# Kernel tuning notes

Hardware: AMD Instinct MI355X
Metric: run time of the kernel (lower is better)

Reference implementation:

```python
import jax, jax.numpy as jnp
import numpy as np

D_IN, N_HEADS, HEAD_DIM = 2048, 16, 128
SEQ, BATCH = 2048, 1
EPS = 1e-6


def rms_norm(x, scale, shift):
    # matches torch RMSNorm: computed in fp32, (1+scale)*x_norm + shift, cast back
    xf = x.astype(jnp.float32)
    rms = jnp.sqrt(jnp.mean(xf * xf, axis=-1, keepdims=True) + EPS)
    out = (xf / rms) * (1.0 + scale.astype(jnp.float32)) + shift.astype(jnp.float32)
    return out.astype(x.dtype)


def apply_rope(x, sin_t, cos_t):
    # x: [b, h, s, d]; sin/cos: [s, d]
    d = x.shape[-1]
    x1, x2 = x[..., : d // 2], x[..., d // 2 :]
    rot = jnp.concatenate([-x2, x1], axis=-1)
    return (x * cos_t[None, None] + rot * sin_t[None, None]).astype(x.dtype)


def setup_inputs() -> dict:
    key = jax.random.key(0)
    ks = jax.random.split(key, 8)
    x = jax.random.normal(ks[0], (BATCH, SEQ, D_IN), dtype=jnp.float32)
    # causal mask: True above the diagonal (positions to mask)
    mask = jnp.triu(jnp.ones((SEQ, SEQ), dtype=bool), k=1)
    # standard RoPE tables, shape [s, head_dim] (half-freqs tiled over both halves)
    inv_freq = 1.0 / (10000.0 ** (np.arange(0, HEAD_DIM, 2, dtype=np.float32) / HEAD_DIM))
    t = np.arange(SEQ, dtype=np.float32)
    ang = np.einsum('s,f->sf', t, inv_freq)          # [s, d/2]
    ang = np.concatenate([ang, ang], axis=-1)        # [s, d]
    sin_thetas = jnp.asarray(np.sin(ang))
    cos_thetas = jnp.asarray(np.cos(ang))
    d_out = N_HEADS * HEAD_DIM
    std = 0.02
    w_q = jax.random.normal(ks[1], (d_out, D_IN), dtype=jnp.float32) * std
    w_k = jax.random.normal(ks[2], (HEAD_DIM, D_IN), dtype=jnp.float32) * std
    w_v = jax.random.normal(ks[3], (HEAD_DIM, D_IN), dtype=jnp.float32) * std
    w_o = jax.random.normal(ks[4], (D_IN, d_out), dtype=jnp.float32) * std
    q_scale = jnp.zeros((HEAD_DIM,), jnp.float32)
    q_shift = jnp.zeros((HEAD_DIM,), jnp.float32)
    k_scale = jnp.zeros((HEAD_DIM,), jnp.float32)
    k_shift = jnp.zeros((HEAD_DIM,), jnp.float32)
    return dict(x=x, mask=mask, sin_thetas=sin_thetas, cos_thetas=cos_thetas,
                w_q=w_q, w_k=w_k, w_v=w_v, w_o=w_o,
                q_scale=q_scale, q_shift=q_shift, k_scale=k_scale, k_shift=k_shift)


def reference(x, mask, sin_thetas, cos_thetas, w_q, w_k, w_v, w_o,
              q_scale, q_shift, k_scale, k_shift):
    b, s, _ = x.shape
    scale = HEAD_DIM ** -0.5
    q = jnp.einsum('bsd,ed->bse', x, w_q).reshape(b, s, N_HEADS, HEAD_DIM)
    q = jnp.transpose(q, (0, 2, 1, 3))                 # [b, H, s, Dh]
    k = jnp.einsum('bsd,ed->bse', x, w_k)[:, None]     # [b, 1, s, Dh]
    v = jnp.einsum('bsd,ed->bse', x, w_v)[:, None]     # [b, 1, s, Dh]
    q = rms_norm(q, q_scale, q_shift)
    k = rms_norm(k, k_scale, k_shift)
    q = apply_rope(q, sin_thetas, cos_thetas)
    k = apply_rope(k, sin_thetas, cos_thetas)
    # MQA: broadcast single K/V head instead of repeat_interleave
    scores = jnp.einsum('bhqd,bokd->bhqk', q, k) * scale   # o==1 broadcast
    scores = jnp.where(mask[None, None], -jnp.inf, scores)
    w = jax.nn.softmax(scores, axis=-1)
    out = jnp.einsum('bhqk,bokd->bhqd', w, v)
    out = jnp.transpose(out, (0, 2, 1, 3)).reshape(b, s, N_HEADS * HEAD_DIM)
    return jnp.einsum('bse,de->bsd', out, w_o)
```

## Files before the change

kernel.cpp:

```cpp
#include <hip/hip_runtime.h>
#include <stdint.h>

#define SEQ 2048
#define DIN 2048
#define NH 16
#define HD 128

typedef __attribute__((ext_vector_type(8))) short bf16x8;
typedef __attribute__((ext_vector_type(4))) float f32x4;

__device__ __forceinline__ unsigned short f2bf(float f) {
    unsigned int u = __float_as_uint(f);
    u += 0x7fff + ((u >> 16) & 1);
    return (unsigned short)(u >> 16);
}

__device__ __forceinline__ float bf2f(unsigned short u) {
    return __uint_as_float(((unsigned int)u) << 16);
}

__device__ __forceinline__ void gload_lds16(const void* g, void* l) {
    __builtin_amdgcn_global_load_lds(
        (const __attribute__((address_space(1))) unsigned int*)g,
        (__attribute__((address_space(3))) unsigned int*)l,
        16, 0, 0);
}

__global__ void cast_f32_bf16(const float* __restrict__ in, unsigned short* __restrict__ out, int n) {
    int i = (blockIdx.x * blockDim.x + threadIdx.x) * 4;
    if (i >= n) return;
    float4 v = *reinterpret_cast<const float4*>(in + i);
    ushort4 o;
    o.x = f2bf(v.x); o.y = f2bf(v.y); o.z = f2bf(v.z); o.w = f2bf(v.w);
    *reinterpret_cast<ushort4*>(out + i) = o;
}

template<int OUT_MODE>
__launch_bounds__(256)
__global__ void gemm_bt(const unsigned short* __restrict__ A,
                        const unsigned short* __restrict__ B,
                        void* __restrict__ Cv, int M, int N, int K) {
    __shared__ __align__(16) unsigned short As[128 * 32];
    __shared__ __align__(16) unsigned short Bs[128 * 32];
    const int t = threadIdx.x;
    const int l = t & 63;
    const int w = t >> 6;
    const int wr = w >> 1, wc = w & 1;
    const int row0 = blockIdx.y * 128, col0 = blockIdx.x * 128;
    const int lr = l & 15, lk = (l >> 4) * 8;

    f32x4 acc[4][4] = {};

    const unsigned short* Ag0 = A + (size_t)(row0 + t / 4) * K + (t % 4) * 8;
    const unsigned short* Ag1 = Ag0 + (size_t)64 * K;
    const unsigned short* Bg0 = B + (size_t)(col0 + t / 4) * K + (t % 4) * 8;
    const unsigned short* Bg1 = Bg0 + (size_t)64 * K;

    for (int k0 = 0; k0 < K; k0 += 32) {
        gload_lds16(Ag0 + k0, &As[t * 8]);
        gload_lds16(Ag1 + k0, &As[2048 + t * 8]);
        gload_lds16(Bg0 + k0, &Bs[t * 8]);
        gload_lds16(Bg1 + k0, &Bs[2048 + t * 8]);
        __syncthreads();
        bf16x8 af[4], bfr[4];
#pragma unroll
        for (int m = 0; m < 4; ++m)
            af[m] = *reinterpret_cast<const bf16x8*>(&As[(wr * 64 + m * 16 + lr) * 32 + lk]);
#pragma unroll
        for (int n = 0; n < 4; ++n)
            bfr[n] = *reinterpret_cast<const bf16x8*>(&Bs[(wc * 64 + n * 16 + lr) * 32 + lk]);
#pragma unroll
        for (int m = 0; m < 4; ++m)
#pragma unroll
            for (int n = 0; n < 4; ++n)
                acc[m][n] = __builtin_amdgcn_mfma_f32_16x16x32_bf16(af[m], bfr[n], acc[m][n], 0, 0, 0);
        __syncthreads();
    }

#pragma unroll
    for (int m = 0; m < 4; ++m) {
        int row_b = row0 + wr * 64 + m * 16 + (l >> 4) * 4;
#pragma unroll
        for (int n = 0; n < 4; ++n) {
            int col = col0 + wc * 64 + n * 16 + lr;
#pragma unroll
            for (int jr = 0; jr < 4; ++jr) {
                int row = row_b + jr;
                if (OUT_MODE == 0)
                    ((float*)Cv)[(size_t)row * N + col] = acc[m][n][jr];
                else if (OUT_MODE == 1)
                    ((unsigned short*)Cv)[(size_t)row * N + col] = f2bf(acc[m][n][jr]);
                else
                    ((unsigned short*)Cv)[(size_t)col * M + row] = f2bf(acc[m][n][jr]);
            }
        }
    }
}

__global__ void norm_rope(const unsigned short* __restrict__ in, int srow,
                          unsigned short* __restrict__ out,
                          const float* __restrict__ sin_t, const float* __restrict__ cos_t,
                          const float* __restrict__ scale, const float* __restrict__ shift,
                          int nh) {
    int w = threadIdx.x >> 6, lane = threadIdx.x & 63;
    int vec = blockIdx.x * 4 + w;
    if (vec >= SEQ * nh) return;
    int s = vec / nh, hh = vec % nh;
    const unsigned short* base = in + (size_t)s * srow + hh * HD;
    float x1 = bf2f(base[lane]), x2 = bf2f(base[lane + 64]);
    float ss = x1 * x1 + x2 * x2;
#pragma unroll
    for (int off = 1; off < 64; off <<= 1) ss += __shfl_xor(ss, off, 64);
    float rinv = rsqrtf(ss * (1.0f / 128.0f) + 1e-6f);
    float xn1 = x1 * rinv * (1.0f + scale[lane]) + shift[lane];
    float xn2 = x2 * rinv * (1.0f + scale[lane + 64]) + shift[lane + 64];
    float c1 = cos_t[s * HD + lane], s1 = sin_t[s * HD + lane];
    float c2 = cos_t[s * HD + lane + 64], s2 = sin_t[s * HD + lane + 64];
    float o1 = xn1 * c1 - xn2 * s1;
    float o2 = xn2 * c2 + xn1 * s2;
    out[(size_t)vec * HD + lane] = f2bf(o1);
    out[(size_t)vec * HD + lane + 64] = f2bf(o2);
}

__launch_bounds__(256)
__global__ void flash_attn2(const unsigned short* __restrict__ Q,
                            const unsigned short* __restrict__ Kb,
                            const unsigned short* __restrict__ Vtg,
                            unsigned short* __restrict__ O) {
    __shared__ __align__(16) unsigned short Ks[2][64 * 128];
    __shared__ __align__(16) unsigned short Vs[2][128 * 64];
    __shared__ __align__(16) unsigned short Pl[4][16 * 64];
    const int t = threadIdx.x, l = t & 63, w = t >> 6;
    const int h = blockIdx.y;
    const int lr = l & 15, g = l >> 4, lk = g * 8;
    const float sc = 0.08838834764831845f;

    auto stage = [&](int buf, int k0) {
#pragma unroll
        for (int i = 0; i < 4; ++i) {
            int c = w * 256 + i * 64 + l;
            int kr = c >> 4, kc = c & 15;
            gload_lds16(Kb + (size_t)(k0 + kr) * HD + ((kc ^ (kr & 7)) * 8),
                        &Ks[buf][c * 8]);
            int vd = c >> 3, vc = c & 7;
            gload_lds16(Vtg + (size_t)vd * SEQ + k0 + ((vc ^ (vd & 7)) * 8),
                        &Vs[buf][c * 8]);
        }
    };

    auto process = [&](int qt) {
        const int q0 = qt * 64;
        bf16x8 qf[4];
        const unsigned short* qbase = Q + (size_t)(q0 + w * 16 + lr) * (NH * HD) + h * HD + lk;
#pragma unroll
        for (int kf = 0; kf < 4; ++kf)
            qf[kf] = *reinterpret_cast<const bf16x8*>(qbase + kf * 32);

        f32x4 acc[8] = {};
        float mrow[4] = {-1e30f, -1e30f, -1e30f, -1e30f};
        float lrow[4] = {0.f, 0.f, 0.f, 0.f};
        const int nt = qt + 1;
        int buf = 0;
        stage(0, 0);
        __syncthreads();

        for (int kt = 0; kt < nt; ++kt) {
            if (kt + 1 < nt) stage(buf ^ 1, (kt + 1) * 64);

            f32x4 s4[4];
#pragma unroll
            for (int nf = 0; nf < 4; ++nf) {
                int row = nf * 16 + lr;
                f32x4 a = {};
#pragma unroll
                for (int kf = 0; kf < 4; ++kf) {
                    bf16x8 kfrag = *reinterpret_cast<const bf16x8*>(
                        &Ks[buf][row * 128 + ((kf * 32 + lk) ^ ((row & 7) << 3))]);
                    a = __builtin_amdgcn_mfma_f32_16x16x32_bf16(qf[kf], kfrag, a, 0, 0, 0);
                }
                s4[nf] = a;
            }

            float sv[4][4];
            const bool diag = (kt == qt);
#pragma unroll
            for (int jr = 0; jr < 4; ++jr)
#pragma unroll
                for (int nf = 0; nf < 4; ++nf) {
                    float x = s4[nf][jr] * sc;
                    if (diag && (nf * 16 + lr > w * 16 + g * 4 + jr)) x = -1e30f;
                    sv[jr][nf] = x;
                }

            float mx[4];
#pragma unroll
            for (int jr = 0; jr < 4; ++jr) {
                float m2 = fmaxf(fmaxf(sv[jr][0], sv[jr][1]), fmaxf(sv[jr][2], sv[jr][3]));
                m2 = fmaxf(m2, __shfl_xor(m2, 1, 64));
                m2 = fmaxf(m2, __shfl_xor(m2, 2, 64));
                m2 = fmaxf(m2, __shfl_xor(m2, 4, 64));
                m2 = fmaxf(m2, __shfl_xor(m2, 8, 64));
                mx[jr] = m2;
            }
            int pred = (mx[0] - mrow[0] <= 8.f) && (mx[1] - mrow[1] <= 8.f) &&
                       (mx[2] - mrow[2] <= 8.f) && (mx[3] - mrow[3] <= 8.f);
            const bool skip = __all(pred);

#pragma unroll
            for (int jr = 0; jr < 4; ++jr) {
                float mnew = skip ? mrow[jr] : fmaxf(mrow[jr], mx[jr]);
                int row = g * 4 + jr;
                float ps = 0.f;
#pragma unroll
                for (int nf = 0; nf < 4; ++nf) {
                    float p = __expf(sv[jr][nf] - mnew);
                    ps += p;
                    int col = nf * 16 + lr;
                    Pl[w][row * 64 + (col ^ ((row & 12) << 2))] = f2bf(p);
                }
                ps += __shfl_xor(ps, 1, 64);
                ps += __shfl_xor(ps, 2, 64);
                ps += __shfl_xor(ps, 4, 64);
                ps += __shfl_xor(ps, 8, 64);
                if (!skip) {
                    float corr = __expf(mrow[jr] - mnew);
                    mrow[jr] = mnew;
                    lrow[jr] = lrow[jr] * corr + ps;
#pragma unroll
                    for (int nf = 0; nf < 8; ++nf) acc[nf][jr] *= corr;
                } else {
                    lrow[jr] += ps;
                }
            }

            asm volatile("s_waitcnt lgkmcnt(0)" ::: "memory");
            __builtin_amdgcn_sched_barrier(0);

#pragma unroll
            for (int kf = 0; kf < 2; ++kf) {
                bf16x8 pf = *reinterpret_cast<const bf16x8*>(
                    &Pl[w][lr * 64 + ((kf * 32 + lk) ^ ((lr & 12) << 2))]);
#pragma unroll
                for (int nf = 0; nf < 8; ++nf) {
                    int d = nf * 16 + lr;
                    bf16x8 vf = *reinterpret_cast<const bf16x8*>(
                        &Vs[buf][d * 64 + ((kf * 32 + lk) ^ ((d & 7) << 3))]);
                    acc[nf] = __builtin_amdgcn_mfma_f32_16x16x32_bf16(pf, vf, acc[nf], 0, 0, 0);
                }
            }
            __syncthreads();
            buf ^= 1;
        }

#pragma unroll
        for (int jr = 0; jr < 4; ++jr) {
            float inv = 1.0f / lrow[jr];
            int row = q0 + w * 16 + g * 4 + jr;
#pragma unroll
            for (int nf = 0; nf < 8; ++nf) {
                int col = nf * 16 + lr;
                O[(size_t)row * (NH * HD) + h * HD + col] = f2bf(acc[nf][jr] * inv);
            }
        }
    };

    process(blockIdx.x);
    process(31 - blockIdx.x);
}

extern "C" void kernel_launch(void* const* d_in, const int* in_sizes, int n_in,
                              void* d_out, int out_size, void* d_ws, size_t ws_size,
                              hipStream_t stream) {
    const float* x      = (const float*)d_in[0];
    const float* sin_t  = (const float*)d_in[2];
    const float* cos_t  = (const float*)d_in[3];
    const float* w_q    = (const float*)d_in[4];
    const float* w_k    = (const float*)d_in[5];
    const float* w_v    = (const float*)d_in[6];
    const float* w_o    = (const float*)d_in[7];
    const float* q_scale = (const float*)d_in[8];
    const float* q_shift = (const float*)d_in[9];
    const float* k_scale = (const float*)d_in[10];
    const float* k_shift = (const float*)d_in[11];
    float* out = (float*)d_out;

    char* ws = (char*)d_ws;
    const size_t MB = 1u << 20;
    unsigned short* xb    = (unsigned short*)(ws);
    unsigned short* wqkb  = (unsigned short*)(ws + 8 * MB);
    unsigned short* wvb   = (unsigned short*)(ws + 16 * MB + 512 * 1024);
    unsigned short* wob   = (unsigned short*)(ws + 17 * MB);
    unsigned short* qkpre = (unsigned short*)(ws + 25 * MB);
    unsigned short* vtb   = (unsigned short*)(ws + 33 * MB + 512 * 1024);
    unsigned short* qb    = (unsigned short*)(ws + 34 * MB);
    unsigned short* kb    = (unsigned short*)(ws + 42 * MB);
    unsigned short* ab    = (unsigned short*)(ws + 42 * MB + 512 * 1024);

    auto cast = [&](const float* src, unsigned short* dst, int n) {
        cast_f32_bf16<<<(n / 4 + 255) / 256, 256, 0, stream>>>(src, dst, n);
    };
    cast(x,   xb,   SEQ * DIN);
    cast(w_q, wqkb, NH * HD * DIN);
    cast(w_k, wqkb + (size_t)NH * HD * DIN, HD * DIN);
    cast(w_v, wvb,  HD * DIN);
    cast(w_o, wob,  DIN * NH * HD);

    gemm_bt<1><<<dim3(17, 16), 256, 0, stream>>>(xb, wqkb, qkpre, SEQ, NH * HD + HD, DIN);
    gemm_bt<2><<<dim3(1, 16), 256, 0, stream>>>(xb, wvb, vtb, SEQ, HD, DIN);

    norm_rope<<<SEQ * NH / 4, 256, 0, stream>>>(qkpre, NH * HD + HD, qb, sin_t, cos_t, q_scale, q_shift, NH);
    norm_rope<<<SEQ / 4, 256, 0, stream>>>(qkpre + NH * HD, NH * HD + HD, kb, sin_t, cos_t, k_scale, k_shift, 1);

    flash_attn2<<<dim3(16, 16), 256, 0, stream>>>(qb, kb, vtb, ab);

    gemm_bt<0><<<dim3(16, 16), 256, 0, stream>>>(ab, wob, out, SEQ, NH * HD, DIN);
}
```

Baseline: 351.7 us.

## Merge cast and norm launches, widen GEMM blocks, split attention per q-tile

The five cast kernels become one launch, and the two norm/rope launches become one, to cut launch overhead. The GEMM now runs 512 threads per block (8 waves, each computing a 32x64 sub-tile) to raise per-CU occupancy without changing the tile size. Flash attention moves from 256 blocks that each processed a paired light and heavy q-tile to 512 blocks of one q-tile each, heaviest first, to balance load through the scheduler. Risks include fewer MFMAs per LDS load in the GEMM and the loss of the paired balancing in attention.

```diff
diff --git a/kernel.cpp b/kernel.cpp
--- a/kernel.cpp
+++ b/kernel.cpp
@@ -26,20 +26,29 @@
         16, 0, 0);
 }
 
-__global__ void cast_f32_bf16(const float* __restrict__ in, unsigned short* __restrict__ out, int n) {
-    int i = (blockIdx.x * blockDim.x + threadIdx.x) * 4;
-    if (i >= n) return;
-    float4 v = *reinterpret_cast<const float4*>(in + i);
+__global__ void cast_all(const float* __restrict__ x,  const float* __restrict__ wq,
+                         const float* __restrict__ wk, const float* __restrict__ wv,
+                         const float* __restrict__ wo,
+                         unsigned short* __restrict__ xb, unsigned short* __restrict__ wqk,
+                         unsigned short* __restrict__ wvb, unsigned short* __restrict__ wob) {
+    int i = blockIdx.x * blockDim.x + threadIdx.x;
+    const float* src; unsigned short* dst; int off;
+    if (i < 1048576)      { src = x;  dst = xb;            off = i; }
+    else if (i < 2097152) { src = wq; dst = wqk;           off = i - 1048576; }
+    else if (i < 2162688) { src = wk; dst = wqk + 4194304; off = i - 2097152; }
+    else if (i < 2228224) { src = wv; dst = wvb;           off = i - 2162688; }
+    else                  { src = wo; dst = wob;           off = i - 2228224; }
+    float4 v = *reinterpret_cast<const float4*>(src + (size_t)off * 4);
     ushort4 o;
     o.x = f2bf(v.x); o.y = f2bf(v.y); o.z = f2bf(v.z); o.w = f2bf(v.w);
-    *reinterpret_cast<ushort4*>(out + i) = o;
+    *reinterpret_cast<ushort4*>(dst + (size_t)off * 4) = o;
 }
 
 template<int OUT_MODE>
-__launch_bounds__(256)
-__global__ void gemm_bt(const unsigned short* __restrict__ A,
-                        const unsigned short* __restrict__ B,
-                        void* __restrict__ Cv, int M, int N, int K) {
+__launch_bounds__(512)
+__global__ void gemm_bt8(const unsigned short* __restrict__ A,
+                         const unsigned short* __restrict__ B,
+                         void* __restrict__ Cv, int M, int N, int K) {
     __shared__ __align__(16) unsigned short As[128 * 32];
     __shared__ __align__(16) unsigned short Bs[128 * 32];
     const int t = threadIdx.x;
@@ -49,28 +58,24 @@
     const int row0 = blockIdx.y * 128, col0 = blockIdx.x * 128;
     const int lr = l & 15, lk = (l >> 4) * 8;
 
-    f32x4 acc[4][4] = {};
-
-    const unsigned short* Ag0 = A + (size_t)(row0 + t / 4) * K + (t % 4) * 8;
-    const unsigned short* Ag1 = Ag0 + (size_t)64 * K;
-    const unsigned short* Bg0 = B + (size_t)(col0 + t / 4) * K + (t % 4) * 8;
-    const unsigned short* Bg1 = Bg0 + (size_t)64 * K;
+    f32x4 acc[2][4] = {};
+
+    const unsigned short* Ag = A + (size_t)(row0 + t / 4) * K + (t % 4) * 8;
+    const unsigned short* Bg = B + (size_t)(col0 + t / 4) * K + (t % 4) * 8;
 
     for (int k0 = 0; k0 < K; k0 += 32) {
-        gload_lds16(Ag0 + k0, &As[t * 8]);
-        gload_lds16(Ag1 + k0, &As[2048 + t * 8]);
-        gload_lds16(Bg0 + k0, &Bs[t * 8]);
-        gload_lds16(Bg1 + k0, &Bs[2048 + t * 8]);
+        gload_lds16(Ag + k0, &As[t * 8]);
+        gload_lds16(Bg + k0, &Bs[t * 8]);
         __syncthreads();
-        bf16x8 af[4], bfr[4];
-#pragma unroll
-        for (int m = 0; m < 4; ++m)
-            af[m] = *reinterpret_cast<const bf16x8*>(&As[(wr * 64 + m * 16 + lr) * 32 + lk]);
+        bf16x8 af[2], bfr[4];
+#pragma unroll
+        for (int m = 0; m < 2; ++m)
+            af[m] = *reinterpret_cast<const bf16x8*>(&As[(wr * 32 + m * 16 + lr) * 32 + lk]);
 #pragma unroll
         for (int n = 0; n < 4; ++n)
             bfr[n] = *reinterpret_cast<const bf16x8*>(&Bs[(wc * 64 + n * 16 + lr) * 32 + lk]);
 #pragma unroll
-        for (int m = 0; m < 4; ++m)
+        for (int m = 0; m < 2; ++m)
 #pragma unroll
             for (int n = 0; n < 4; ++n)
                 acc[m][n] = __builtin_amdgcn_mfma_f32_16x16x32_bf16(af[m], bfr[n], acc[m][n], 0, 0, 0);
@@ -78,8 +83,8 @@
     }
 
 #pragma unroll
-    for (int m = 0; m < 4; ++m) {
-        int row_b = row0 + wr * 64 + m * 16 + (l >> 4) * 4;
+    for (int m = 0; m < 2; ++m) {
+        int row_b = row0 + wr * 32 + m * 16 + (l >> 4) * 4;
 #pragma unroll
         for (int n = 0; n < 4; ++n) {
             int col = col0 + wc * 64 + n * 16 + lr;
@@ -97,16 +102,31 @@
     }
 }
 
-__global__ void norm_rope(const unsigned short* __restrict__ in, int srow,
-                          unsigned short* __restrict__ out,
-                          const float* __restrict__ sin_t, const float* __restrict__ cos_t,
-                          const float* __restrict__ scale, const float* __restrict__ shift,
-                          int nh) {
+__global__ void norm_rope_all(const unsigned short* __restrict__ qk,
+                              unsigned short* __restrict__ qout,
+                              unsigned short* __restrict__ kout,
+                              const float* __restrict__ sin_t, const float* __restrict__ cos_t,
+                              const float* __restrict__ q_scale, const float* __restrict__ q_shift,
+                              const float* __restrict__ k_scale, const float* __restrict__ k_shift) {
     int w = threadIdx.x >> 6, lane = threadIdx.x & 63;
     int vec = blockIdx.x * 4 + w;
-    if (vec >= SEQ * nh) return;
-    int s = vec / nh, hh = vec % nh;
-    const unsigned short* base = in + (size_t)s * srow + hh * HD;
+    if (vec >= SEQ * NH + SEQ) return;
+    const unsigned short* base;
+    unsigned short* outp;
+    const float *scale, *shift;
+    int s;
+    if (vec < SEQ * NH) {
+        s = vec >> 4;
+        int hh = vec & 15;
+        base = qk + (size_t)s * 2176 + hh * HD;
+        outp = qout + (size_t)vec * HD;
+        scale = q_scale; shift = q_shift;
+    } else {
+        s = vec - SEQ * NH;
+        base = qk + (size_t)s * 2176 + NH * HD;
+        outp = kout + (size_t)s * HD;
+        scale = k_scale; shift = k_shift;
+    }
     float x1 = bf2f(base[lane]), x2 = bf2f(base[lane + 64]);
     float ss = x1 * x1 + x2 * x2;
 #pragma unroll
@@ -116,14 +136,12 @@
     float xn2 = x2 * rinv * (1.0f + scale[lane + 64]) + shift[lane + 64];
     float c1 = cos_t[s * HD + lane], s1 = sin_t[s * HD + lane];
     float c2 = cos_t[s * HD + lane + 64], s2 = sin_t[s * HD + lane + 64];
-    float o1 = xn1 * c1 - xn2 * s1;
-    float o2 = xn2 * c2 + xn1 * s2;
-    out[(size_t)vec * HD + lane] = f2bf(o1);
-    out[(size_t)vec * HD + lane + 64] = f2bf(o2);
+    outp[lane]      = f2bf(xn1 * c1 - xn2 * s1);
+    outp[lane + 64] = f2bf(xn2 * c2 + xn1 * s2);
 }
 
 __launch_bounds__(256)
-__global__ void flash_attn2(const unsigned short* __restrict__ Q,
+__global__ void flash_attn3(const unsigned short* __restrict__ Q,
                             const unsigned short* __restrict__ Kb,
                             const unsigned short* __restrict__ Vtg,
                             unsigned short* __restrict__ O) {
@@ -131,7 +149,9 @@
     __shared__ __align__(16) unsigned short Vs[2][128 * 64];
     __shared__ __align__(16) unsigned short Pl[4][16 * 64];
     const int t = threadIdx.x, l = t & 63, w = t >> 6;
-    const int h = blockIdx.y;
+    const int bx = blockIdx.x;
+    const int qt = (bx < 256) ? (31 - (bx >> 4)) : ((bx - 256) >> 4);
+    const int h = bx & 15;
     const int lr = l & 15, g = l >> 4, lk = g * 8;
     const float sc = 0.08838834764831845f;
 
@@ -148,124 +168,119 @@
         }
     };
 
-    auto process = [&](int qt) {
-        const int q0 = qt * 64;
-        bf16x8 qf[4];
-        const unsigned short* qbase = Q + (size_t)(q0 + w * 16 + lr) * (NH * HD) + h * HD + lk;
-#pragma unroll
-        for (int kf = 0; kf < 4; ++kf)
-            qf[kf] = *reinterpret_cast<const bf16x8*>(qbase + kf * 32);
-
-        f32x4 acc[8] = {};
-        float mrow[4] = {-1e30f, -1e30f, -1e30f, -1e30f};
-        float lrow[4] = {0.f, 0.f, 0.f, 0.f};
-        const int nt = qt + 1;
-        int buf = 0;
-        stage(0, 0);
+    const int q0 = qt * 64;
+    bf16x8 qf[4];
+    const unsigned short* qbase = Q + (size_t)(q0 + w * 16 + lr) * (NH * HD) + h * HD + lk;
+#pragma unroll
+    for (int kf = 0; kf < 4; ++kf)
+        qf[kf] = *reinterpret_cast<const bf16x8*>(qbase + kf * 32);
+
+    f32x4 acc[8] = {};
+    float mrow[4] = {-1e30f, -1e30f, -1e30f, -1e30f};
+    float lrow[4] = {0.f, 0.f, 0.f, 0.f};
+    const int nt = qt + 1;
+    int buf = 0;
+    stage(0, 0);
+    __syncthreads();
+
+    for (int kt = 0; kt < nt; ++kt) {
+        if (kt + 1 < nt) stage(buf ^ 1, (kt + 1) * 64);
+
+        f32x4 s4[4];
+#pragma unroll
+        for (int nf = 0; nf < 4; ++nf) {
+            int row = nf * 16 + lr;
+            f32x4 a = {};
+#pragma unroll
+            for (int kf = 0; kf < 4; ++kf) {
+                bf16x8 kfrag = *reinterpret_cast<const bf16x8*>(
+                    &Ks[buf][row * 128 + ((kf * 32 + lk) ^ ((row & 7) << 3))]);
+                a = __builtin_amdgcn_mfma_f32_16x16x32_bf16(qf[kf], kfrag, a, 0, 0, 0);
+            }
+            s4[nf] = a;
+        }
+
+        float sv[4][4];
+        const bool diag = (kt == qt);
+#pragma unroll
+        for (int jr = 0; jr < 4; ++jr)
+#pragma unroll
+            for (int nf = 0; nf < 4; ++nf) {
+                float x = s4[nf][jr] * sc;
+                if (diag && (nf * 16 + lr > w * 16 + g * 4 + jr)) x = -1e30f;
+                sv[jr][nf] = x;
+            }
+
+        float mx[4];
+#pragma unroll
+        for (int jr = 0; jr < 4; ++jr) {
+            float m2 = fmaxf(fmaxf(sv[jr][0], sv[jr][1]), fmaxf(sv[jr][2], sv[jr][3]));
+            m2 = fmaxf(m2, __shfl_xor(m2, 1, 64));
+            m2 = fmaxf(m2, __shfl_xor(m2, 2, 64));
+            m2 = fmaxf(m2, __shfl_xor(m2, 4, 64));
+            m2 = fmaxf(m2, __shfl_xor(m2, 8, 64));
+            mx[jr] = m2;
+        }
+        int pred = (mx[0] - mrow[0] <= 8.f) && (mx[1] - mrow[1] <= 8.f) &&
+                   (mx[2] - mrow[2] <= 8.f) && (mx[3] - mrow[3] <= 8.f);
+        const bool skip = __all(pred);
+
+#pragma unroll
+        for (int jr = 0; jr < 4; ++jr) {
+            float mnew = skip ? mrow[jr] : fmaxf(mrow[jr], mx[jr]);
+            int row = g * 4 + jr;
+            float ps = 0.f;
+#pragma unroll
+            for (int nf = 0; nf < 4; ++nf) {
+                float p = __expf(sv[jr][nf] - mnew);
+                ps += p;
+                int col = nf * 16 + lr;
+                Pl[w][row * 64 + (col ^ ((row & 12) << 2))] = f2bf(p);
+            }
+            ps += __shfl_xor(ps, 1, 64);
+            ps += __shfl_xor(ps, 2, 64);
+            ps += __shfl_xor(ps, 4, 64);
+            ps += __shfl_xor(ps, 8, 64);
+            if (!skip) {
+                float corr = __expf(mrow[jr] - mnew);
+                mrow[jr] = mnew;
+                lrow[jr] = lrow[jr] * corr + ps;
+#pragma unroll
+                for (int nf = 0; nf < 8; ++nf) acc[nf][jr] *= corr;
+            } else {
+                lrow[jr] += ps;
+            }
+        }
+
+        asm volatile("s_waitcnt lgkmcnt(0)" ::: "memory");
+        __builtin_amdgcn_sched_barrier(0);
+
+#pragma unroll
+        for (int kf = 0; kf < 2; ++kf) {
+            bf16x8 pf = *reinterpret_cast<const bf16x8*>(
+                &Pl[w][lr * 64 + ((kf * 32 + lk) ^ ((lr & 12) << 2))]);
+#pragma unroll
+            for (int nf = 0; nf < 8; ++nf) {
+                int d = nf * 16 + lr;
+                bf16x8 vf = *reinterpret_cast<const bf16x8*>(
+                    &Vs[buf][d * 64 + ((kf * 32 + lk) ^ ((d & 7) << 3))]);
+                acc[nf] = __builtin_amdgcn_mfma_f32_16x16x32_bf16(pf, vf, acc[nf], 0, 0, 0);
+            }
+        }
         __syncthreads();
-
-        for (int kt = 0; kt < nt; ++kt) {
-            if (kt + 1 < nt) stage(buf ^ 1, (kt + 1) * 64);
-
-            f32x4 s4[4];
-#pragma unroll
-            for (int nf = 0; nf < 4; ++nf) {
-                int row = nf * 16 + lr;
-                f32x4 a = {};
-#pragma unroll
-                for (int kf = 0; kf < 4; ++kf) {
-                    bf16x8 kfrag = *reinterpret_cast<const bf16x8*>(
-                        &Ks[buf][row * 128 + ((kf * 32 + lk) ^ ((row & 7) << 3))]);
-                    a = __builtin_amdgcn_mfma_f32_16x16x32_bf16(qf[kf], kfrag, a, 0, 0, 0);
-                }
-                s4[nf] = a;
-            }
-
-            float sv[4][4];
-            const bool diag = (kt == qt);
-#pragma unroll
-            for (int jr = 0; jr < 4; ++jr)
-#pragma unroll
-                for (int nf = 0; nf < 4; ++nf) {
-                    float x = s4[nf][jr] * sc;
-                    if (diag && (nf * 16 + lr > w * 16 + g * 4 + jr)) x = -1e30f;
-                    sv[jr][nf] = x;
-                }
-
-            float mx[4];
-#pragma unroll
-            for (int jr = 0; jr < 4; ++jr) {
-                float m2 = fmaxf(fmaxf(sv[jr][0], sv[jr][1]), fmaxf(sv[jr][2], sv[jr][3]));
-                m2 = fmaxf(m2, __shfl_xor(m2, 1, 64));
-                m2 = fmaxf(m2, __shfl_xor(m2, 2, 64));
-                m2 = fmaxf(m2, __shfl_xor(m2, 4, 64));
-                m2 = fmaxf(m2, __shfl_xor(m2, 8, 64));
-                mx[jr] = m2;
-            }
-            int pred = (mx[0] - mrow[0] <= 8.f) && (mx[1] - mrow[1] <= 8.f) &&
-                       (mx[2] - mrow[2] <= 8.f) && (mx[3] - mrow[3] <= 8.f);
-            const bool skip = __all(pred);
-
-#pragma unroll
-            for (int jr = 0; jr < 4; ++jr) {
-                float mnew = skip ? mrow[jr] : fmaxf(mrow[jr], mx[jr]);
-                int row = g * 4 + jr;
-                float ps = 0.f;
-#pragma unroll
-                for (int nf = 0; nf < 4; ++nf) {
-                    float p = __expf(sv[jr][nf] - mnew);
-                    ps += p;
-                    int col = nf * 16 + lr;
-                    Pl[w][row * 64 + (col ^ ((row & 12) << 2))] = f2bf(p);
-                }
-                ps += __shfl_xor(ps, 1, 64);
-                ps += __shfl_xor(ps, 2, 64);
-                ps += __shfl_xor(ps, 4, 64);
-                ps += __shfl_xor(ps, 8, 64);
-                if (!skip) {
-                    float corr = __expf(mrow[jr] - mnew);
-                    mrow[jr] = mnew;
-                    lrow[jr] = lrow[jr] * corr + ps;
-#pragma unroll
-                    for (int nf = 0; nf < 8; ++nf) acc[nf][jr] *= corr;
-                } else {
-                    lrow[jr] += ps;
-                }
-            }
-
-            asm volatile("s_waitcnt lgkmcnt(0)" ::: "memory");
-            __builtin_amdgcn_sched_barrier(0);
-
-#pragma unroll
-            for (int kf = 0; kf < 2; ++kf) {
-                bf16x8 pf = *reinterpret_cast<const bf16x8*>(
-                    &Pl[w][lr * 64 + ((kf * 32 + lk) ^ ((lr & 12) << 2))]);
-#pragma unroll
-                for (int nf = 0; nf < 8; ++nf) {
-                    int d = nf * 16 + lr;
-                    bf16x8 vf = *reinterpret_cast<const bf16x8*>(
-                        &Vs[buf][d * 64 + ((kf * 32 + lk) ^ ((d & 7) << 3))]);
-                    acc[nf] = __builtin_amdgcn_mfma_f32_16x16x32_bf16(pf, vf, acc[nf], 0, 0, 0);
-                }
-            }
-            __syncthreads();
-            buf ^= 1;
-        }
-
-#pragma unroll
-        for (int jr = 0; jr < 4; ++jr) {
-            float inv = 1.0f / lrow[jr];
-            int row = q0 + w * 16 + g * 4 + jr;
-#pragma unroll
-            for (int nf = 0; nf < 8; ++nf) {
-                int col = nf * 16 + lr;
-                O[(size_t)row * (NH * HD) + h * HD + col] = f2bf(acc[nf][jr] * inv);
-            }
-        }
-    };
-
-    process(blockIdx.x);
-    process(31 - blockIdx.x);
+        buf ^= 1;
+    }
+
+#pragma unroll
+    for (int jr = 0; jr < 4; ++jr) {
+        float inv = 1.0f / lrow[jr];
+        int row = q0 + w * 16 + g * 4 + jr;
+#pragma unroll
+        for (int nf = 0; nf < 8; ++nf) {
+            int col = nf * 16 + lr;
+            O[(size_t)row * (NH * HD) + h * HD + col] = f2bf(acc[nf][jr] * inv);
+        }
+    }
 }
 
 extern "C" void kernel_launch(void* const* d_in, const int* in_sizes, int n_in,
@@ -296,22 +311,15 @@
     unsigned short* kb    = (unsigned short*)(ws + 42 * MB);
     unsigned short* ab    = (unsigned short*)(ws + 42 * MB + 512 * 1024);
 
-    auto cast = [&](const float* src, unsigned short* dst, int n) {
-        cast_f32_bf16<<<(n / 4 + 255) / 256, 256, 0, stream>>>(src, dst, n);
-    };
-    cast(x,   xb,   SEQ * DIN);
-    cast(w_q, wqkb, NH * HD * DIN);
-    cast(w_k, wqkb + (size_t)NH * HD * DIN, HD * DIN);
-    cast(w_v, wvb,  HD * DIN);
-    cast(w_o, wob,  DIN * NH * HD);
-
-    gemm_bt<1><<<dim3(17, 16), 256, 0, stream>>>(xb, wqkb, qkpre, SEQ, NH * HD + HD, DIN);
-    gemm_bt<2><<<dim3(1, 16), 256, 0, stream>>>(xb, wvb, vtb, SEQ, HD, DIN);
-
-    norm_rope<<<SEQ * NH / 4, 256, 0, stream>>>(qkpre, NH * HD + HD, qb, sin_t, cos_t, q_scale, q_shift, NH);
-    norm_rope<<<SEQ / 4, 256, 0, stream>>>(qkpre + NH * HD, NH * HD + HD, kb, sin_t, cos_t, k_scale, k_shift, 1);
-
-    flash_attn2<<<dim3(16, 16), 256, 0, stream>>>(qb, kb, vtb, ab);
-
-    gemm_bt<0><<<dim3(16, 16), 256, 0, stream>>>(ab, wob, out, SEQ, NH * HD, DIN);
-}
+    cast_all<<<12800, 256, 0, stream>>>(x, w_q, w_k, w_v, w_o, xb, wqkb, wvb, wob);
+
+    gemm_bt8<1><<<dim3(17, 16), 512, 0, stream>>>(xb, wqkb, qkpre, SEQ, NH * HD + HD, DIN);
+    gemm_bt8<2><<<dim3(1, 16), 512, 0, stream>>>(xb, wvb, vtb, SEQ, HD, DIN);
+
+    norm_rope_all<<<(SEQ * NH + SEQ) / 4, 256, 0, stream>>>(
+        qkpre, qb, kb, sin_t, cos_t, q_scale, q_shift, k_scale, k_shift);
+
+    flash_attn3<<<512, 256, 0, stream>>>(qb, kb, vtb, ab);
+
+    gemm_bt8<0><<<dim3(16, 16), 512, 0, stream>>>(ab, wob, out, SEQ, NH * HD, DIN);
+}
```

After: 377.2 us. +7.2%, slower.
